# Kernel optimization log

Measured on AMD Instinct MI355X. Metric: run time of the kernel, lower is better.

The kernel has to match this reference:

```python
import jax, jax.numpy as jnp
import numpy as np
import itertools


def _comb_indices(F, k):
    # Flattened combination indices: for each of C(F,k) combinations, its k
    # member feature ids, concatenated. Row i of the original one-hot crmatrix
    # has a single 1 at column idx[i], so x @ crmatrix^T == gather by idx.
    return np.fromiter(itertools.chain(*itertools.combinations(range(F), k)),
                       dtype=np.int32)


def setup_inputs() -> dict:
    key = jax.random.key(0)
    x = jax.random.normal(key, (32, 4096, 32), dtype=jnp.float32)  # [B, T, F]
    return {"x": x, "k": 2}


def reference(x, k):
    F = x.shape[2]
    idx = jnp.asarray(_comb_indices(F, k))          # [ncr] = [k * C(F,k)]
    # Faithful to K.dot(x, crmatrix) with one-hot crmatrix: a feature gather.
    return jnp.take(x, idx, axis=2)                 # [B, T, ncr]
```

## Files before the change

### kernel.cpp

```cpp
#include <hip/hip_runtime.h>


#define FDIM 32
#define NCR 992
#define G_PER_ROW 248
#define ROWS_PER_BLOCK 16
#define BLOCK 256

typedef float f32x4 __attribute__((ext_vector_type(4)));
typedef float f32x2 __attribute__((ext_vector_type(2)));

__global__ __launch_bounds__(BLOCK)
void comb_gather_kernel(const float* __restrict__ x,
                        float* __restrict__ out,
                        int nrows) {
    __shared__ float lds[ROWS_PER_BLOCK * FDIM];

    const int tid  = threadIdx.x;
    const int row0 = blockIdx.x * ROWS_PER_BLOCK;
    const bool full = (row0 + ROWS_PER_BLOCK) <= nrows;

    {
        const f32x2* src = reinterpret_cast<const f32x2*>(x + (size_t)row0 * FDIM);
        if (full) {
            reinterpret_cast<f32x2*>(lds)[tid] = src[tid];
        } else {
            int row_of_load = row0 + (tid * 2) / FDIM;
            if (row_of_load < nrows)
                reinterpret_cast<f32x2*>(lds)[tid] = src[tid];
        }
    }

    int feat[4];
    const int g = tid;
    if (g < G_PER_ROW) {
        const int c0 = 2 * g;
        float s = sqrtf(3969.0f - 8.0f * (float)c0);
        int i0 = (int)((63.0f - s) * 0.5f);
        if (i0 < 0) i0 = 0;
        int st0  = (i0 * (63 - i0)) >> 1;
        int stn0 = ((i0 + 1) * (62 - i0)) >> 1;
        if (stn0 <= c0) { i0++; st0 = stn0; stn0 = ((i0 + 1) * (62 - i0)) >> 1; }
        else if (st0 > c0) { i0--; stn0 = st0; st0 = (i0 * (63 - i0)) >> 1; }
        feat[0] = i0;
        feat[1] = c0 - st0 + i0 + 1;
        const int c1 = c0 + 1;
        int i1 = i0, st1 = st0;
        if (stn0 <= c1) { i1 = i0 + 1; st1 = stn0; }
        feat[2] = i1;
        feat[3] = c1 - st1 + i1 + 1;
    }
    __syncthreads();

    if (g >= G_PER_ROW) return;

    if (full) {
        f32x4* outp = reinterpret_cast<f32x4*>(out + (size_t)row0 * NCR) + g;
        #pragma unroll
        for (int r = 0; r < ROWS_PER_BLOCK; ++r) {
            const float* rowp = lds + r * FDIM;
            f32x4 v;
            v.x = rowp[feat[0]];
            v.y = rowp[feat[1]];
            v.z = rowp[feat[2]];
            v.w = rowp[feat[3]];
            __builtin_nontemporal_store(v, outp);
            outp += NCR / 4;
        }
    } else {
        #pragma unroll
        for (int r = 0; r < ROWS_PER_BLOCK; ++r) {
            int row = row0 + r;
            if (row >= nrows) break;
            const float* rowp = lds + r * FDIM;
            f32x4 v;
            v.x = rowp[feat[0]];
            v.y = rowp[feat[1]];
            v.z = rowp[feat[2]];
            v.w = rowp[feat[3]];
            __builtin_nontemporal_store(
                v, reinterpret_cast<f32x4*>(out + (size_t)row * NCR) + g);
        }
    }
}

extern "C" void kernel_launch(void* const* d_in, const int* in_sizes, int n_in,
                              void* d_out, int out_size, void* d_ws, size_t ws_size,
                              hipStream_t stream) {
    const float* x  = (const float*)d_in[0];
    float* out      = (float*)d_out;
    int nrows = in_sizes[0] / FDIM;
    int grid  = (nrows + ROWS_PER_BLOCK - 1) / ROWS_PER_BLOCK;
    hipLaunchKernelGGL(comb_gather_kernel, dim3(grid), dim3(BLOCK), 0, stream,
                       x, out, nrows);
}
```

Baseline: 101.1 us.

## Use persistent blocks with double-buffered LDS tile loads for comb gather

Launches a fixed grid of 512 blocks that each loop over a contiguous range of 16-row tiles instead of one block per tile. The next tile's input is prefetched into registers and written into a second LDS buffer while the current tile's outputs are stored, aiming to hide input load latency and block launch overhead. It lowers the number of resident waves, which may reduce the store parallelism available to this write-bound kernel.

```diff
diff --git a/kernel.cpp b/kernel.cpp
--- a/kernel.cpp
+++ b/kernel.cpp
@@ -4,8 +4,9 @@
 #define FDIM 32
 #define NCR 992
 #define G_PER_ROW 248
-#define ROWS_PER_BLOCK 16
+#define TROWS 16
 #define BLOCK 256
+#define GRID 512
 
 typedef float f32x4 __attribute__((ext_vector_type(4)));
 typedef float f32x2 __attribute__((ext_vector_type(2)));
@@ -14,26 +15,18 @@
 void comb_gather_kernel(const float* __restrict__ x,
                         float* __restrict__ out,
                         int nrows) {
-    __shared__ float lds[ROWS_PER_BLOCK * FDIM];
+    __shared__ float lds[2][TROWS * FDIM];
 
-    const int tid  = threadIdx.x;
-    const int row0 = blockIdx.x * ROWS_PER_BLOCK;
-    const bool full = (row0 + ROWS_PER_BLOCK) <= nrows;
-
-    {
-        const f32x2* src = reinterpret_cast<const f32x2*>(x + (size_t)row0 * FDIM);
-        if (full) {
-            reinterpret_cast<f32x2*>(lds)[tid] = src[tid];
-        } else {
-            int row_of_load = row0 + (tid * 2) / FDIM;
-            if (row_of_load < nrows)
-                reinterpret_cast<f32x2*>(lds)[tid] = src[tid];
-        }
-    }
+    const int tid = threadIdx.x;
+    const int tiles_total = (nrows + TROWS - 1) / TROWS;
+    const int tpb = (tiles_total + (int)gridDim.x - 1) / (int)gridDim.x;
+    const int t0  = blockIdx.x * tpb;
+    const int t1  = (t0 + tpb < tiles_total) ? (t0 + tpb) : tiles_total;
+    if (t0 >= t1) return;
 
     int feat[4];
-    const int g = tid;
-    if (g < G_PER_ROW) {
+    {
+        const int g  = (tid < G_PER_ROW) ? tid : 0;
         const int c0 = 2 * g;
         float s = sqrtf(3969.0f - 8.0f * (float)c0);
         int i0 = (int)((63.0f - s) * 0.5f);
@@ -50,37 +43,65 @@
         feat[2] = i1;
         feat[3] = c1 - st1 + i1 + 1;
     }
+
+    const size_t xtot = (size_t)nrows * FDIM;
+
+    auto load_tile = [&](int t) -> f32x2 {
+        size_t base = (size_t)t * (TROWS * FDIM) + 2 * tid;
+        f32x2 v; v.x = 0.f; v.y = 0.f;
+        if (base + 1 < xtot) v = *reinterpret_cast<const f32x2*>(x + base);
+        else if (base < xtot) v.x = x[base];
+        return v;
+    };
+
+    {
+        f32x2 cur = load_tile(t0);
+        reinterpret_cast<f32x2*>(lds[0])[tid] = cur;
+    }
     __syncthreads();
 
-    if (g >= G_PER_ROW) return;
+    int buf = 0;
+    for (int t = t0; t < t1; ++t) {
+        f32x2 nxt;
+        const bool havenext = (t + 1 < t1);
+        if (havenext) nxt = load_tile(t + 1);
 
-    if (full) {
-        f32x4* outp = reinterpret_cast<f32x4*>(out + (size_t)row0 * NCR) + g;
-        #pragma unroll
-        for (int r = 0; r < ROWS_PER_BLOCK; ++r) {
-            const float* rowp = lds + r * FDIM;
-            f32x4 v;
-            v.x = rowp[feat[0]];
-            v.y = rowp[feat[1]];
-            v.z = rowp[feat[2]];
-            v.w = rowp[feat[3]];
-            __builtin_nontemporal_store(v, outp);
-            outp += NCR / 4;
+        if (tid < G_PER_ROW) {
+            const int g = tid;
+            const float* L = lds[buf];
+            const int rbeg = t * TROWS;
+            const int rcnt = (nrows - rbeg < TROWS) ? (nrows - rbeg) : TROWS;
+            f32x4* outp = reinterpret_cast<f32x4*>(out + (size_t)rbeg * NCR) + g;
+            if (rcnt == TROWS) {
+                #pragma unroll
+                for (int r = 0; r < TROWS; ++r) {
+                    const float* rowp = L + r * FDIM;
+                    f32x4 v;
+                    v.x = rowp[feat[0]];
+                    v.y = rowp[feat[1]];
+                    v.z = rowp[feat[2]];
+                    v.w = rowp[feat[3]];
+                    __builtin_nontemporal_store(v, outp);
+                    outp += NCR / 4;
+                }
+            } else {
+                for (int r = 0; r < rcnt; ++r) {
+                    const float* rowp = L + r * FDIM;
+                    f32x4 v;
+                    v.x = rowp[feat[0]];
+                    v.y = rowp[feat[1]];
+                    v.z = rowp[feat[2]];
+                    v.w = rowp[feat[3]];
+                    __builtin_nontemporal_store(v, outp);
+                    outp += NCR / 4;
+                }
+            }
         }
-    } else {
-        #pragma unroll
-        for (int r = 0; r < ROWS_PER_BLOCK; ++r) {
-            int row = row0 + r;
-            if (row >= nrows) break;
-            const float* rowp = lds + r * FDIM;
-            f32x4 v;
-            v.x = rowp[feat[0]];
-            v.y = rowp[feat[1]];
-            v.z = rowp[feat[2]];
-            v.w = rowp[feat[3]];
-            __builtin_nontemporal_store(
-                v, reinterpret_cast<f32x4*>(out + (size_t)row * NCR) + g);
-        }
+
+        if (havenext)
+            reinterpret_cast<f32x2*>(lds[buf ^ 1])[tid] = nxt;
+        __syncthreads();
+        buf ^= 1;
     }
 }
 
@@ -90,7 +111,6 @@
     const float* x  = (const float*)d_in[0];
     float* out      = (float*)d_out;
     int nrows = in_sizes[0] / FDIM;
-    int grid  = (nrows + ROWS_PER_BLOCK - 1) / ROWS_PER_BLOCK;
-    hipLaunchKernelGGL(comb_gather_kernel, dim3(grid), dim3(BLOCK), 0, stream,
+    hipLaunchKernelGGL(comb_gather_kernel, dim3(GRID), dim3(BLOCK), 0, stream,
                        x, out, nrows);
 }
```

Measured after the change: 110.6 us. 9.5% more time.
